# Performance work log

Hardware: AMD Instinct MI355X
Metric: run time of the kernel (lower is better)

## Reference

```python
import jax, jax.numpy as jnp
import numpy as np

B, S, D, H = 2, 2048, 1024, 16
DK = D // H
NEG = -1000000000.0


def setup_inputs() -> dict:
    key = jax.random.key(0)
    ks = jax.random.split(key, 12)
    s = 1.0 / np.sqrt(D)
    return {
        "Q": jax.random.normal(ks[0], (B, S, D), jnp.float32),
        "K": jax.random.normal(ks[1], (B, S, D), jnp.float32),
        "V": jax.random.normal(ks[2], (B, S, D), jnp.float32),
        "attn_mask": jnp.zeros((B, S, S), jnp.bool_),
        "WQ_w": jax.random.normal(ks[3], (D, D), jnp.float32) * s,
        "WQ_b": jnp.zeros((D,), jnp.float32),
        "WK_w": jax.random.normal(ks[4], (D, D), jnp.float32) * s,
        "WK_b": jnp.zeros((D,), jnp.float32),
        "WV_w": jax.random.normal(ks[5], (D, D), jnp.float32) * s,
        "WV_b": jnp.zeros((D,), jnp.float32),
        "fc_w": jax.random.normal(ks[6], (D, D), jnp.float32) * s,
        "fc_b": jnp.zeros((D,), jnp.float32),
    }


def reference(Q, K, V, attn_mask, WQ_w, WQ_b, WK_w, WK_b, WV_w, WV_b, fc_w, fc_b):
    b = Q.shape[0]
    # linear projections (torch Linear: x @ W^T + b), split heads -> [b, h, s, dk]
    q = (Q @ WQ_w.T + WQ_b).reshape(b, -1, H, DK).transpose(0, 2, 1, 3)
    k = (K @ WK_w.T + WK_b).reshape(b, -1, H, DK).transpose(0, 2, 1, 3)
    v = (V @ WV_w.T + WV_b).reshape(b, -1, H, DK).transpose(0, 2, 1, 3)
    # scaled dot-product attention with masked_fill
    scores = jnp.einsum("bhqd,bhkd->bhqk", q, k) / jnp.sqrt(jnp.float32(DK))
    scores = jnp.where(attn_mask[:, None, :, :], NEG, scores)
    attn_weights = jax.nn.softmax(scores, axis=-1)  # dropout p=0 -> identity
    attn = jnp.einsum("bhqk,bhkd->bhqd", attn_weights, v)
    attn = attn.transpose(0, 2, 1, 3).reshape(b, -1, H * DK)
    output = attn @ fc_w.T + fc_b
    return output, attn_weights
```

## Files before the change

kernel.cpp:

```cpp
#include <hip/hip_runtime.h>
#include <cstdint>
#include <cstddef>

constexpr int CB = 2;
constexpr int CS = 2048;
constexpr int CD = 1024;
constexpr int CH = 16;
constexpr int CDK = 64;
constexpr float NEGV = -1000000000.0f;
constexpr float QSCALE = 0.18033688011112042f;

typedef __bf16 bf16x8 __attribute__((ext_vector_type(8)));
typedef float f32x4 __attribute__((ext_vector_type(4)));
typedef unsigned short u16x8 __attribute__((ext_vector_type(8)));
typedef unsigned short u16x4 __attribute__((ext_vector_type(4)));

static __device__ __forceinline__ unsigned short f2bf(float x) {
  unsigned int u = __float_as_uint(x);
  u += 0x7fffu + ((u >> 16) & 1u);
  return (unsigned short)(u >> 16);
}
static __device__ __forceinline__ bf16x8 bc8(u16x8 u) {
  return __builtin_bit_cast(bf16x8, u);
}
static __device__ __forceinline__ f32x4 mfma16(bf16x8 a, bf16x8 b, f32x4 c) {
  return __builtin_amdgcn_mfma_f32_16x16x32_bf16(a, b, c, 0, 0, 0);
}

struct CvtArgs {
  const float* src[7];
  unsigned short* dst[7];
  int n4[7];
};

__global__ __launch_bounds__(256) void cvt_all(CvtArgs a) {
  const int r = blockIdx.y;
  const float* __restrict__ in = a.src[r];
  unsigned short* __restrict__ out = a.dst[r];
  const int n4 = a.n4[r];
  const int stride = gridDim.x * 256;
  for (int i = blockIdx.x * 256 + threadIdx.x; i < n4; i += stride) {
    float4 v = reinterpret_cast<const float4*>(in)[i];
    u16x4 o;
    o[0] = f2bf(v.x); o[1] = f2bf(v.y); o[2] = f2bf(v.z); o[3] = f2bf(v.w);
    reinterpret_cast<u16x4*>(out)[i] = o;
  }
}

constexpr int GK = 1024, GNT = GK / 32;

struct QKVArgs {
  const unsigned short* X[3];
  const unsigned short* W[3];
  const float* bias[3];
  unsigned short* out[3];
  float osc[3];
};

template <typename EPI>
__device__ __forceinline__ void gemm_body(const unsigned short* __restrict__ X,
                                          const unsigned short* __restrict__ Wt,
                                          EPI epi) {
  __shared__ unsigned short lA[2][128 * 32];
  __shared__ unsigned short lB[2][64 * 32];
  const int tid = threadIdx.x, lane = tid & 63, wid = tid >> 6;
  const int fr = lane & 15, fc = lane >> 4;
  const int mbase = blockIdx.y * 128, nbase = blockIdx.x * 64;
  const int wm = (wid & 1) * 64, wn = (wid >> 1) * 32;

  const int srow = wid * 16 + (lane >> 2);
  const int sslot = (lane & 3) ^ (srow & 3);
  const unsigned short* a0 = X + (size_t)(mbase + srow) * GK + sslot * 8;
  const unsigned short* b0 = Wt + (size_t)(nbase + srow) * GK + sslot * 8;

  auto stage = [&](int buf, int k0) {
    __builtin_amdgcn_global_load_lds(
        (const __attribute__((address_space(1))) void*)(a0 + k0),
        (__attribute__((address_space(3))) void*)((char*)&lA[buf][0] + wid * 1024), 16, 0, 0);
    __builtin_amdgcn_global_load_lds(
        (const __attribute__((address_space(1))) void*)(a0 + (size_t)64 * GK + k0),
        (__attribute__((address_space(3))) void*)((char*)&lA[buf][0] + 4096 + wid * 1024), 16, 0, 0);
    __builtin_amdgcn_global_load_lds(
        (const __attribute__((address_space(1))) void*)(b0 + k0),
        (__attribute__((address_space(3))) void*)((char*)&lB[buf][0] + wid * 1024), 16, 0, 0);
  };

  f32x4 acc[4][2] = {};
  stage(0, 0);
  __syncthreads();
  for (int t = 0; t < GNT; ++t) {
    if (t + 1 < GNT) stage((t + 1) & 1, (t + 1) * 32);
    const int buf = t & 1;
    bf16x8 af[4], bfv[2];
#pragma unroll
    for (int i = 0; i < 4; ++i) {
      const int row = wm + i * 16 + fr;
      af[i] = bc8(*reinterpret_cast<const u16x8*>(&lA[buf][row * 32 + ((fc ^ (row & 3)) * 8)]));
    }
#pragma unroll
    for (int j = 0; j < 2; ++j) {
      const int row = wn + j * 16 + fr;
      bfv[j] = bc8(*reinterpret_cast<const u16x8*>(&lB[buf][row * 32 + ((fc ^ (row & 3)) * 8)]));
    }
#pragma unroll
    for (int i = 0; i < 4; ++i)
#pragma unroll
      for (int j = 0; j < 2; ++j)
        acc[i][j] = mfma16(af[i], bfv[j], acc[i][j]);
    __syncthreads();
  }

#pragma unroll
  for (int j = 0; j < 2; ++j) {
    const int colb = nbase + wn + j * 16 + fr;
#pragma unroll
    for (int i = 0; i < 4; ++i) {
#pragma unroll
      for (int r = 0; r < 4; ++r) {
        const int rowb = mbase + wm + i * 16 + fc * 4 + r;
        epi(rowb, colb, acc[i][j][r]);
      }
    }
  }
}

__global__ __launch_bounds__(256) void gemm_qkv(QKVArgs a) {
  const int z = blockIdx.z;
  const float* bias = a.bias[z];
  unsigned short* out = a.out[z];
  const float osc = a.osc[z];
  gemm_body(a.X[z], a.W[z], [&](int rowb, int colb, float av) {
    const float v = (av + bias[colb]) * osc;
    const int bb = rowb >> 11, sr = rowb & (CS - 1);
    const int hh = colb >> 6, cc = colb & (CDK - 1);
    const size_t bh = (size_t)bb * CH + hh;
    if (z == 0) {
      out[(bh * CS + sr) * CDK + cc] = f2bf(v);
    } else if (z == 1) {
      const int kt = sr >> 6, ww = sr & 63, g = ww >> 4, fr2 = ww & 15;
      const int half = cc >> 5, fc2 = (cc >> 3) & 3, zz = cc & 7;
      out[(bh * 256 + kt * 8 + g * 2 + half) * 512 + (fc2 * 16 + fr2) * 8 + zz] = f2bf(v);
    } else {
      const int kt = sr >> 6, ww = sr & 63, c2 = ww >> 5, fc2 = (ww >> 3) & 3, zz = ww & 7;
      const int g = cc >> 4, fr2 = cc & 15;
      out[(bh * 256 + kt * 8 + g * 2 + c2) * 512 + (fc2 * 16 + fr2) * 8 + zz] = f2bf(v);
    }
  });
}

__global__ __launch_bounds__(256) void gemm_fc(const unsigned short* __restrict__ X,
                                               const unsigned short* __restrict__ Wt,
                                               const float* __restrict__ bias,
                                               float* __restrict__ out) {
  gemm_body(X, Wt, [&](int rowb, int colb, float av) {
    out[(size_t)rowb * CD + colb] = av + bias[colb];
  });
}

constexpr int WLD = 68;

__global__ __launch_bounds__(256, 3) void attn_fused(const unsigned short* __restrict__ qh,
                                                     const unsigned short* __restrict__ kT,
                                                     const unsigned short* __restrict__ vT,
                                                     const unsigned char* __restrict__ mask,
                                                     float* __restrict__ attnw,
                                                     unsigned short* __restrict__ attn_pre) {
  __shared__ float lW[4][16 * WLD];

  const int tid = threadIdx.x, lane = tid & 63, wid = tid >> 6;
  const int bid = blockIdx.x;
  const int swz = (bid & 7) * 128 + (bid >> 3);
  const int qt = swz & 31, hh = (swz >> 5) & 15, b = swz >> 9;
  const int bh = b * CH + hh;
  const int qw = qt * 64 + wid * 16;
  const int fr = lane & 15, fc = lane >> 4;

  const unsigned short* qp = qh + ((size_t)bh * CS + qw + fr) * CDK + fc * 8;
  const bf16x8 aq0 = bc8(*reinterpret_cast<const u16x8*>(qp));
  const bf16x8 aq1 = bc8(*reinterpret_cast<const u16x8*>(qp + 32));

  const unsigned short* kbase = kT + (size_t)bh * 131072 + lane * 8;
  const unsigned short* vbase = vT + (size_t)bh * 131072 + lane * 8;

  const unsigned char* mrow = mask + ((size_t)b * CS + qw + (lane >> 2)) * CS + (lane & 3) * 16;
  unsigned int dirtybits = 0;
#pragma unroll 4
  for (int kt = 0; kt < 32; ++kt) {
    const uint4 mv = *reinterpret_cast<const uint4*>(mrow + kt * 64);
    if (__ballot((mv.x | mv.y | mv.z | mv.w) != 0)) dirtybits |= (1u << kt);
  }

  u16x8 kreg[8];
  auto loadK = [&](int kt) {
    const unsigned short* p = kbase + (size_t)kt * 4096;
#pragma unroll
    for (int f = 0; f < 8; ++f) kreg[f] = *reinterpret_cast<const u16x8*>(p + f * 512);
  };
  auto maskfix = [&](f32x4 (&sf)[4], int kt) {
#pragma unroll
    for (int g = 0; g < 4; ++g)
#pragma unroll
      for (int r = 0; r < 4; ++r) {
        const unsigned char mb =
            mask[((size_t)b * CS + qw + fc * 4 + r) * CS + kt * 64 + g * 16 + fr];
        if (mb) sf[g][r] = NEGV;
      }
  };

  float l_r[4] = {0.f, 0.f, 0.f, 0.f};
  loadK(0);
  for (int kt = 0; kt < 32; ++kt) {
    f32x4 sf[4];
#pragma unroll
    for (int g = 0; g < 4; ++g) {
      f32x4 a = {0.f, 0.f, 0.f, 0.f};
      a = mfma16(aq0, bc8(kreg[2 * g]), a);
      a = mfma16(aq1, bc8(kreg[2 * g + 1]), a);
      sf[g] = a;
    }
    loadK(kt + 1 < 32 ? kt + 1 : 0);
    if ((dirtybits >> kt) & 1u) maskfix(sf, kt);
#pragma unroll
    for (int r = 0; r < 4; ++r)
      l_r[r] += exp2f(sf[0][r]) + exp2f(sf[1][r]) + exp2f(sf[2][r]) + exp2f(sf[3][r]);
  }

  float linv[4];
#pragma unroll
  for (int r = 0; r < 4; ++r) {
    float s = l_r[r];
    s += __shfl_xor(s, 1);
    s += __shfl_xor(s, 2);
    s += __shfl_xor(s, 4);
    s += __shfl_xor(s, 8);
    linv[r] = 1.0f / s;
  }

  f32x4 o[4] = {};
  u16x8 vreg[8];
  auto loadV = [&](int kt) {
    const unsigned short* p = vbase + (size_t)kt * 4096;
#pragma unroll
    for (int f = 0; f < 8; ++f) vreg[f] = *reinterpret_cast<const u16x8*>(p + f * 512);
  };
  loadK(0);
  for (int kt = 0; kt < 32; ++kt) {
    loadV(kt);

    f32x4 sf[4];
#pragma unroll
    for (int g = 0; g < 4; ++g) {
      f32x4 a = {0.f, 0.f, 0.f, 0.f};
      a = mfma16(aq0, bc8(kreg[2 * g]), a);
      a = mfma16(aq1, bc8(kreg[2 * g + 1]), a);
      sf[g] = a;
    }
    loadK(kt + 1 < 32 ? kt + 1 : 0);
    if ((dirtybits >> kt) & 1u) maskfix(sf, kt);

#pragma unroll
    for (int g = 0; g < 4; ++g)
#pragma unroll
      for (int r = 0; r < 4; ++r) sf[g][r] = exp2f(sf[g][r]) * linv[r];

#pragma unroll
    for (int g = 0; g < 4; ++g)
#pragma unroll
      for (int r = 0; r < 4; ++r)
        lW[wid][(fc * 4 + r) * WLD + g * 16 + fr] = sf[g][r];

#pragma unroll
    for (int it = 0; it < 4; ++it) {
      const int row = it * 4 + fc;
      const f32x4 wv = *reinterpret_cast<const f32x4*>(&lW[wid][row * WLD + fr * 4]);
      __builtin_nontemporal_store(
          wv, reinterpret_cast<f32x4*>(
                  &attnw[((size_t)bh * CS + qw + row) * CS + kt * 64 + fr * 4]));
    }

    bf16x8 wa[2];
#pragma unroll
    for (int c = 0; c < 2; ++c) {
      const f32x4 t0 = *reinterpret_cast<const f32x4*>(&lW[wid][fr * WLD + c * 32 + fc * 8]);
      const f32x4 t1 = *reinterpret_cast<const f32x4*>(&lW[wid][fr * WLD + c * 32 + fc * 8 + 4]);
      unsigned int w0, w1, w2, w3;
      asm("v_cvt_pk_bf16_f32 %0, %1, %2" : "=v"(w0) : "v"(t0[0]), "v"(t0[1]));
      asm("v_cvt_pk_bf16_f32 %0, %1, %2" : "=v"(w1) : "v"(t0[2]), "v"(t0[3]));
      asm("v_cvt_pk_bf16_f32 %0, %1, %2" : "=v"(w2) : "v"(t1[0]), "v"(t1[1]));
      asm("v_cvt_pk_bf16_f32 %0, %1, %2" : "=v"(w3) : "v"(t1[2]), "v"(t1[3]));
      uint4 uw = {w0, w1, w2, w3};
      wa[c] = __builtin_bit_cast(bf16x8, uw);
    }
#pragma unroll
    for (int g = 0; g < 4; ++g) {
      o[g] = mfma16(wa[0], bc8(vreg[2 * g]), o[g]);
      o[g] = mfma16(wa[1], bc8(vreg[2 * g + 1]), o[g]);
    }
  }

#pragma unroll
  for (int g = 0; g < 4; ++g)
#pragma unroll
    for (int r = 0; r < 4; ++r) {
      const int q = qw + fc * 4 + r;
      attn_pre[(((size_t)b * CS + q) * CH + hh) * CDK + g * 16 + fr] = f2bf(o[g][r]);
    }
}

extern "C" void kernel_launch(void* const* d_in, const int* in_sizes, int n_in,
                              void* d_out, int out_size, void* d_ws, size_t ws_size,
                              hipStream_t stream) {
  (void)in_sizes; (void)n_in; (void)out_size; (void)ws_size;

  const float* Qf = (const float*)d_in[0];
  const float* Kf = (const float*)d_in[1];
  const float* Vf = (const float*)d_in[2];
  const unsigned char* mask = (const unsigned char*)d_in[3];
  const float* WQw = (const float*)d_in[4];
  const float* WQb = (const float*)d_in[5];
  const float* WKw = (const float*)d_in[6];
  const float* WKb = (const float*)d_in[7];
  const float* WVw = (const float*)d_in[8];
  const float* WVb = (const float*)d_in[9];
  const float* fcw = (const float*)d_in[10];
  const float* fcb = (const float*)d_in[11];

  float* out0 = (float*)d_out;
  float* attnw = out0 + (size_t)CB * CS * CD;

  char* w = (char*)d_ws;
  unsigned short* Qb = (unsigned short*)(w);
  unsigned short* Kb = (unsigned short*)(w + 8388608);
  unsigned short* Vb = (unsigned short*)(w + 2 * 8388608);
  unsigned short* Wqb = (unsigned short*)(w + 3 * 8388608);
  unsigned short* Wkb = Wqb + 1048576;
  unsigned short* Wvb = Wkb + 1048576;
  unsigned short* Wfb = Wvb + 1048576;
  unsigned short* qhp = (unsigned short*)(w + 3 * 8388608 + 4 * 2097152);
  unsigned short* kTp = qhp + 4194304;
  unsigned short* vTp = kTp + 4194304;
  unsigned short* apre = Qb;

  const int NELEM4 = (CB * CS * CD) / 4;
  const int WELEM4 = (CD * CD) / 4;

  CvtArgs ca;
  ca.src[0] = Qf;  ca.dst[0] = Qb;  ca.n4[0] = NELEM4;
  ca.src[1] = Kf;  ca.dst[1] = Kb;  ca.n4[1] = NELEM4;
  ca.src[2] = Vf;  ca.dst[2] = Vb;  ca.n4[2] = NELEM4;
  ca.src[3] = WQw; ca.dst[3] = Wqb; ca.n4[3] = WELEM4;
  ca.src[4] = WKw; ca.dst[4] = Wkb; ca.n4[4] = WELEM4;
  ca.src[5] = WVw; ca.dst[5] = Wvb; ca.n4[5] = WELEM4;
  ca.src[6] = fcw; ca.dst[6] = Wfb; ca.n4[6] = WELEM4;
  cvt_all<<<dim3(512, 7), 256, 0, stream>>>(ca);

  QKVArgs qa;
  qa.X[0] = Qb;  qa.W[0] = Wqb; qa.bias[0] = WQb; qa.out[0] = qhp; qa.osc[0] = QSCALE;
  qa.X[1] = Kb;  qa.W[1] = Wkb; qa.bias[1] = WKb; qa.out[1] = kTp; qa.osc[1] = 1.0f;
  qa.X[2] = Vb;  qa.W[2] = Wvb; qa.bias[2] = WVb; qa.out[2] = vTp; qa.osc[2] = 1.0f;
  gemm_qkv<<<dim3(CD / 64, (CB * CS) / 128, 3), 256, 0, stream>>>(qa);

  attn_fused<<<dim3(1024), 256, 0, stream>>>(qhp, kTp, vTp, mask, attnw, apre);

  gemm_fc<<<dim3(CD / 64, (CB * CS) / 128), 256, 0, stream>>>(apre, Wfb, fcb, out0);
}
```

Measured before the change: 257.2 us.

## Share K/V tiles across waves via double-buffered LDS with direct global-to-LDS loads

Each of the four waves previously loaded the full K and V tiles from global memory into registers on its own. Now the block cooperatively stages each 64-key K/V tile into double-buffered shared memory using global_load_lds. That cuts redundant global and L2 traffic by four and frees registers. The change adds __syncthreads per iteration, s_setprio around the MFMA sections, and 32 KB more LDS, which may reduce occupancy below the launch bound of 3 blocks.

```diff
diff --git a/kernel.cpp b/kernel.cpp
--- a/kernel.cpp
+++ b/kernel.cpp
@@ -165,6 +165,8 @@
                                                      const unsigned char* __restrict__ mask,
                                                      float* __restrict__ attnw,
                                                      unsigned short* __restrict__ attn_pre) {
+  __shared__ unsigned short lK[2][4096];
+  __shared__ unsigned short lV[2][4096];
   __shared__ float lW[4][16 * WLD];
 
   const int tid = threadIdx.x, lane = tid & 63, wid = tid >> 6;
@@ -179,8 +181,29 @@
   const bf16x8 aq0 = bc8(*reinterpret_cast<const u16x8*>(qp));
   const bf16x8 aq1 = bc8(*reinterpret_cast<const u16x8*>(qp + 32));
 
-  const unsigned short* kbase = kT + (size_t)bh * 131072 + lane * 8;
-  const unsigned short* vbase = vT + (size_t)bh * 131072 + lane * 8;
+  const unsigned short* kt0 = kT + (size_t)bh * 131072;
+  const unsigned short* vt0 = vT + (size_t)bh * 131072;
+
+  auto stageK = [&](int buf, int kt) {
+    const unsigned short* p = kt0 + (size_t)kt * 4096;
+#pragma unroll
+    for (int cc = 0; cc < 2; ++cc) {
+      const int ch = wid * 2 + cc;
+      __builtin_amdgcn_global_load_lds(
+          (const __attribute__((address_space(1))) void*)(p + ch * 512 + lane * 8),
+          (__attribute__((address_space(3))) void*)(&lK[buf][ch * 512]), 16, 0, 0);
+    }
+  };
+  auto stageV = [&](int buf, int kt) {
+    const unsigned short* p = vt0 + (size_t)kt * 4096;
+#pragma unroll
+    for (int cc = 0; cc < 2; ++cc) {
+      const int ch = wid * 2 + cc;
+      __builtin_amdgcn_global_load_lds(
+          (const __attribute__((address_space(1))) void*)(p + ch * 512 + lane * 8),
+          (__attribute__((address_space(3))) void*)(&lV[buf][ch * 512]), 16, 0, 0);
+    }
+  };
 
   const unsigned char* mrow = mask + ((size_t)b * CS + qw + (lane >> 2)) * CS + (lane & 3) * 16;
   unsigned int dirtybits = 0;
@@ -190,12 +213,6 @@
     if (__ballot((mv.x | mv.y | mv.z | mv.w) != 0)) dirtybits |= (1u << kt);
   }
 
-  u16x8 kreg[8];
-  auto loadK = [&](int kt) {
-    const unsigned short* p = kbase + (size_t)kt * 4096;
-#pragma unroll
-    for (int f = 0; f < 8; ++f) kreg[f] = *reinterpret_cast<const u16x8*>(p + f * 512);
-  };
   auto maskfix = [&](f32x4 (&sf)[4], int kt) {
 #pragma unroll
     for (int g = 0; g < 4; ++g)
@@ -208,21 +225,29 @@
   };
 
   float l_r[4] = {0.f, 0.f, 0.f, 0.f};
-  loadK(0);
+  stageK(0, 0);
+  __syncthreads();
   for (int kt = 0; kt < 32; ++kt) {
+    if (kt < 31) stageK((kt + 1) & 1, kt + 1);
+    const int buf = kt & 1;
     f32x4 sf[4];
+    __builtin_amdgcn_s_setprio(1);
 #pragma unroll
     for (int g = 0; g < 4; ++g) {
+      const bf16x8 k0 = bc8(*reinterpret_cast<const u16x8*>(&lK[buf][(2 * g) * 512 + lane * 8]));
+      const bf16x8 k1 =
+          bc8(*reinterpret_cast<const u16x8*>(&lK[buf][(2 * g + 1) * 512 + lane * 8]));
       f32x4 a = {0.f, 0.f, 0.f, 0.f};
-      a = mfma16(aq0, bc8(kreg[2 * g]), a);
-      a = mfma16(aq1, bc8(kreg[2 * g + 1]), a);
+      a = mfma16(aq0, k0, a);
+      a = mfma16(aq1, k1, a);
       sf[g] = a;
     }
-    loadK(kt + 1 < 32 ? kt + 1 : 0);
+    __builtin_amdgcn_s_setprio(0);
     if ((dirtybits >> kt) & 1u) maskfix(sf, kt);
 #pragma unroll
     for (int r = 0; r < 4; ++r)
-      l_r[r] += exp2f(sf[0][r]) + exp2f(sf[1][r]) + exp2f(sf[2][r]) + exp2f(sf[3][r]);
+      l_r[r] += (exp2f(sf[0][r]) + exp2f(sf[1][r])) + (exp2f(sf[2][r]) + exp2f(sf[3][r]));
+    __syncthreads();
   }
 
   float linv[4];
@@ -237,25 +262,29 @@
   }
 
   f32x4 o[4] = {};
-  u16x8 vreg[8];
-  auto loadV = [&](int kt) {
-    const unsigned short* p = vbase + (size_t)kt * 4096;
-#pragma unroll
-    for (int f = 0; f < 8; ++f) vreg[f] = *reinterpret_cast<const u16x8*>(p + f * 512);
-  };
-  loadK(0);
+  stageK(0, 0);
+  stageV(0, 0);
+  __syncthreads();
   for (int kt = 0; kt < 32; ++kt) {
-    loadV(kt);
+    if (kt < 31) {
+      stageK((kt + 1) & 1, kt + 1);
+      stageV((kt + 1) & 1, kt + 1);
+    }
+    const int buf = kt & 1;
 
     f32x4 sf[4];
+    __builtin_amdgcn_s_setprio(1);
 #pragma unroll
     for (int g = 0; g < 4; ++g) {
+      const bf16x8 k0 = bc8(*reinterpret_cast<const u16x8*>(&lK[buf][(2 * g) * 512 + lane * 8]));
+      const bf16x8 k1 =
+          bc8(*reinterpret_cast<const u16x8*>(&lK[buf][(2 * g + 1) * 512 + lane * 8]));
       f32x4 a = {0.f, 0.f, 0.f, 0.f};
-      a = mfma16(aq0, bc8(kreg[2 * g]), a);
-      a = mfma16(aq1, bc8(kreg[2 * g + 1]), a);
+      a = mfma16(aq0, k0, a);
+      a = mfma16(aq1, k1, a);
       sf[g] = a;
     }
-    loadK(kt + 1 < 32 ? kt + 1 : 0);
+    __builtin_amdgcn_s_setprio(0);
     if ((dirtybits >> kt) & 1u) maskfix(sf, kt);
 
 #pragma unroll
@@ -291,11 +320,17 @@
       uint4 uw = {w0, w1, w2, w3};
       wa[c] = __builtin_bit_cast(bf16x8, uw);
     }
+    __builtin_amdgcn_s_setprio(1);
 #pragma unroll
     for (int g = 0; g < 4; ++g) {
-      o[g] = mfma16(wa[0], bc8(vreg[2 * g]), o[g]);
-      o[g] = mfma16(wa[1], bc8(vreg[2 * g + 1]), o[g]);
-    }
+      const bf16x8 v0 = bc8(*reinterpret_cast<const u16x8*>(&lV[buf][(2 * g) * 512 + lane * 8]));
+      const bf16x8 v1 =
+          bc8(*reinterpret_cast<const u16x8*>(&lV[buf][(2 * g + 1) * 512 + lane * 8]));
+      o[g] = mfma16(wa[0], v0, o[g]);
+      o[g] = mfma16(wa[1], v1, o[g]);
+    }
+    __builtin_amdgcn_s_setprio(0);
+    __syncthreads();
   }
 
 #pragma unroll
```

New measurement: 286.9 us. 11.5% more time.

## Double query rows per attention wave and widen QKV GEMM tile to 128

Applied to the files above, without the earlier changes.

The attention kernel now processes two 16-row query groups per wave, so each K and V fragment loaded from global memory is reused for 32 query rows, and the grid is halved to 512 blocks. Occupancy is relaxed from 3 to 2 blocks per CU to make room for the extra registers. Separately, the QKV projection GEMM becomes templated on the N tile and uses 128-wide tiles, halving its grid and raising per-block reuse of the A tile. The costs are higher register pressure and fewer resident waves to hide latency in both kernels.

```diff
diff --git a/kernel.cpp b/kernel.cpp
--- a/kernel.cpp
+++ b/kernel.cpp
@@ -57,61 +57,72 @@
   float osc[3];
 };
 
-template <typename EPI>
+template <int BN, typename EPI>
 __device__ __forceinline__ void gemm_body(const unsigned short* __restrict__ X,
                                           const unsigned short* __restrict__ Wt,
                                           EPI epi) {
   __shared__ unsigned short lA[2][128 * 32];
-  __shared__ unsigned short lB[2][64 * 32];
+  __shared__ unsigned short lB[2][BN * 32];
   const int tid = threadIdx.x, lane = tid & 63, wid = tid >> 6;
   const int fr = lane & 15, fc = lane >> 4;
-  const int mbase = blockIdx.y * 128, nbase = blockIdx.x * 64;
-  const int wm = (wid & 1) * 64, wn = (wid >> 1) * 32;
-
-  const int srow = wid * 16 + (lane >> 2);
+  const int mbase = blockIdx.y * 128, nbase = blockIdx.x * BN;
+  const int wm = (wid & 1) * 64, wn = (wid >> 1) * (BN / 2);
+
+  const int srow = lane >> 2;
   const int sslot = (lane & 3) ^ (srow & 3);
-  const unsigned short* a0 = X + (size_t)(mbase + srow) * GK + sslot * 8;
-  const unsigned short* b0 = Wt + (size_t)(nbase + srow) * GK + sslot * 8;
+  const int cA = wid * 2;
+  const unsigned short* a0 = X + (size_t)(mbase + cA * 16 + srow) * GK + sslot * 8;
+  const unsigned short* b0;
+  if constexpr (BN == 128) b0 = Wt + (size_t)(nbase + cA * 16 + srow) * GK + sslot * 8;
+  else                     b0 = Wt + (size_t)(nbase + wid * 16 + srow) * GK + sslot * 8;
 
   auto stage = [&](int buf, int k0) {
-    __builtin_amdgcn_global_load_lds(
-        (const __attribute__((address_space(1))) void*)(a0 + k0),
-        (__attribute__((address_space(3))) void*)((char*)&lA[buf][0] + wid * 1024), 16, 0, 0);
-    __builtin_amdgcn_global_load_lds(
-        (const __attribute__((address_space(1))) void*)(a0 + (size_t)64 * GK + k0),
-        (__attribute__((address_space(3))) void*)((char*)&lA[buf][0] + 4096 + wid * 1024), 16, 0, 0);
-    __builtin_amdgcn_global_load_lds(
-        (const __attribute__((address_space(1))) void*)(b0 + k0),
-        (__attribute__((address_space(3))) void*)((char*)&lB[buf][0] + wid * 1024), 16, 0, 0);
-  };
-
-  f32x4 acc[4][2] = {};
+#pragma unroll
+    for (int c = 0; c < 2; ++c)
+      __builtin_amdgcn_global_load_lds(
+          (const __attribute__((address_space(1))) void*)(a0 + (size_t)c * 16 * GK + k0),
+          (__attribute__((address_space(3))) void*)((char*)&lA[buf][0] + (cA + c) * 1024), 16, 0, 0);
+    if constexpr (BN == 128) {
+#pragma unroll
+      for (int c = 0; c < 2; ++c)
+        __builtin_amdgcn_global_load_lds(
+            (const __attribute__((address_space(1))) void*)(b0 + (size_t)c * 16 * GK + k0),
+            (__attribute__((address_space(3))) void*)((char*)&lB[buf][0] + (cA + c) * 1024), 16, 0, 0);
+    } else {
+      __builtin_amdgcn_global_load_lds(
+          (const __attribute__((address_space(1))) void*)(b0 + k0),
+          (__attribute__((address_space(3))) void*)((char*)&lB[buf][0] + wid * 1024), 16, 0, 0);
+    }
+  };
+
+  constexpr int NJ = BN / 32;
+  f32x4 acc[4][NJ] = {};
   stage(0, 0);
   __syncthreads();
   for (int t = 0; t < GNT; ++t) {
     if (t + 1 < GNT) stage((t + 1) & 1, (t + 1) * 32);
     const int buf = t & 1;
-    bf16x8 af[4], bfv[2];
+    bf16x8 af[4], bfv[NJ];
 #pragma unroll
     for (int i = 0; i < 4; ++i) {
       const int row = wm + i * 16 + fr;
       af[i] = bc8(*reinterpret_cast<const u16x8*>(&lA[buf][row * 32 + ((fc ^ (row & 3)) * 8)]));
     }
 #pragma unroll
-    for (int j = 0; j < 2; ++j) {
+    for (int j = 0; j < NJ; ++j) {
       const int row = wn + j * 16 + fr;
       bfv[j] = bc8(*reinterpret_cast<const u16x8*>(&lB[buf][row * 32 + ((fc ^ (row & 3)) * 8)]));
     }
 #pragma unroll
     for (int i = 0; i < 4; ++i)
 #pragma unroll
-      for (int j = 0; j < 2; ++j)
+      for (int j = 0; j < NJ; ++j)
         acc[i][j] = mfma16(af[i], bfv[j], acc[i][j]);
     __syncthreads();
   }
 
 #pragma unroll
-  for (int j = 0; j < 2; ++j) {
+  for (int j = 0; j < NJ; ++j) {
     const int colb = nbase + wn + j * 16 + fr;
 #pragma unroll
     for (int i = 0; i < 4; ++i) {
@@ -124,12 +135,12 @@
   }
 }
 
-__global__ __launch_bounds__(256) void gemm_qkv(QKVArgs a) {
+__global__ __launch_bounds__(256, 3) void gemm_qkv(QKVArgs a) {
   const int z = blockIdx.z;
   const float* bias = a.bias[z];
   unsigned short* out = a.out[z];
   const float osc = a.osc[z];
-  gemm_body(a.X[z], a.W[z], [&](int rowb, int colb, float av) {
+  gemm_body<128>(a.X[z], a.W[z], [&](int rowb, int colb, float av) {
     const float v = (av + bias[colb]) * osc;
     const int bb = rowb >> 11, sr = rowb & (CS - 1);
     const int hh = colb >> 6, cc = colb & (CDK - 1);
@@ -152,14 +163,14 @@
                                                const unsigned short* __restrict__ Wt,
                                                const float* __restrict__ bias,
                                                float* __restrict__ out) {
-  gemm_body(X, Wt, [&](int rowb, int colb, float av) {
+  gemm_body<64>(X, Wt, [&](int rowb, int colb, float av) {
     out[(size_t)rowb * CD + colb] = av + bias[colb];
   });
 }
 
 constexpr int WLD = 68;
 
-__global__ __launch_bounds__(256, 3) void attn_fused(const unsigned short* __restrict__ qh,
+__global__ __launch_bounds__(256, 2) void attn_fused(const unsigned short* __restrict__ qh,
                                                      const unsigned short* __restrict__ kT,
                                                      const unsigned short* __restrict__ vT,
                                                      const unsigned char* __restrict__ mask,
@@ -169,25 +180,32 @@
 
   const int tid = threadIdx.x, lane = tid & 63, wid = tid >> 6;
   const int bid = blockIdx.x;
-  const int swz = (bid & 7) * 128 + (bid >> 3);
-  const int qt = swz & 31, hh = (swz >> 5) & 15, b = swz >> 9;
+  const int swz = (bid & 7) * 64 + (bid >> 3);
+  const int qt = swz & 15, hh = (swz >> 4) & 15, b = swz >> 8;
   const int bh = b * CH + hh;
-  const int qw = qt * 64 + wid * 16;
+  const int qwA = qt * 128 + wid * 32;
+  const int qwB = qwA + 16;
   const int fr = lane & 15, fc = lane >> 4;
 
-  const unsigned short* qp = qh + ((size_t)bh * CS + qw + fr) * CDK + fc * 8;
-  const bf16x8 aq0 = bc8(*reinterpret_cast<const u16x8*>(qp));
-  const bf16x8 aq1 = bc8(*reinterpret_cast<const u16x8*>(qp + 32));
+  const unsigned short* qpA = qh + ((size_t)bh * CS + qwA + fr) * CDK + fc * 8;
+  const bf16x8 aqA0 = bc8(*reinterpret_cast<const u16x8*>(qpA));
+  const bf16x8 aqA1 = bc8(*reinterpret_cast<const u16x8*>(qpA + 32));
+  const unsigned short* qpB = qpA + 16 * CDK;
+  const bf16x8 aqB0 = bc8(*reinterpret_cast<const u16x8*>(qpB));
+  const bf16x8 aqB1 = bc8(*reinterpret_cast<const u16x8*>(qpB + 32));
 
   const unsigned short* kbase = kT + (size_t)bh * 131072 + lane * 8;
   const unsigned short* vbase = vT + (size_t)bh * 131072 + lane * 8;
 
-  const unsigned char* mrow = mask + ((size_t)b * CS + qw + (lane >> 2)) * CS + (lane & 3) * 16;
+  const unsigned char* mrowA = mask + ((size_t)b * CS + qwA + (lane >> 2)) * CS + (lane & 3) * 16;
+  const unsigned char* mrowB = mrowA + (size_t)16 * CS;
   unsigned int dirtybits = 0;
 #pragma unroll 4
   for (int kt = 0; kt < 32; ++kt) {
-    const uint4 mv = *reinterpret_cast<const uint4*>(mrow + kt * 64);
-    if (__ballot((mv.x | mv.y | mv.z | mv.w) != 0)) dirtybits |= (1u << kt);
+    const uint4 m0 = *reinterpret_cast<const uint4*>(mrowA + kt * 64);
+    const uint4 m1 = *reinterpret_cast<const uint4*>(mrowB + kt * 64);
+    if (__ballot((m0.x | m0.y | m0.z | m0.w | m1.x | m1.y | m1.z | m1.w) != 0))
+      dirtybits |= (1u << kt);
   }
 
   u16x8 kreg[8];
@@ -196,7 +214,16 @@
 #pragma unroll
     for (int f = 0; f < 8; ++f) kreg[f] = *reinterpret_cast<const u16x8*>(p + f * 512);
   };
-  auto maskfix = [&](f32x4 (&sf)[4], int kt) {
+  auto qk = [&](const bf16x8 a0, const bf16x8 a1, f32x4 (&sf)[4]) {
+#pragma unroll
+    for (int g = 0; g < 4; ++g) {
+      f32x4 a = {0.f, 0.f, 0.f, 0.f};
+      a = mfma16(a0, bc8(kreg[2 * g]), a);
+      a = mfma16(a1, bc8(kreg[2 * g + 1]), a);
+      sf[g] = a;
+    }
+  };
+  auto maskfix = [&](f32x4 (&sf)[4], int kt, int qw) {
 #pragma unroll
     for (int g = 0; g < 4; ++g)
 #pragma unroll
@@ -207,68 +234,51 @@
       }
   };
 
-  float l_r[4] = {0.f, 0.f, 0.f, 0.f};
+  float lAr[4] = {0.f, 0.f, 0.f, 0.f}, lBr[4] = {0.f, 0.f, 0.f, 0.f};
   loadK(0);
   for (int kt = 0; kt < 32; ++kt) {
-    f32x4 sf[4];
-#pragma unroll
-    for (int g = 0; g < 4; ++g) {
-      f32x4 a = {0.f, 0.f, 0.f, 0.f};
-      a = mfma16(aq0, bc8(kreg[2 * g]), a);
-      a = mfma16(aq1, bc8(kreg[2 * g + 1]), a);
-      sf[g] = a;
-    }
+    f32x4 sfA[4], sfB[4];
+    qk(aqA0, aqA1, sfA);
+    qk(aqB0, aqB1, sfB);
     loadK(kt + 1 < 32 ? kt + 1 : 0);
-    if ((dirtybits >> kt) & 1u) maskfix(sf, kt);
-#pragma unroll
-    for (int r = 0; r < 4; ++r)
-      l_r[r] += exp2f(sf[0][r]) + exp2f(sf[1][r]) + exp2f(sf[2][r]) + exp2f(sf[3][r]);
-  }
-
-  float linv[4];
+    if ((dirtybits >> kt) & 1u) { maskfix(sfA, kt, qwA); maskfix(sfB, kt, qwB); }
+#pragma unroll
+    for (int r = 0; r < 4; ++r) {
+      lAr[r] += (exp2f(sfA[0][r]) + exp2f(sfA[1][r])) + (exp2f(sfA[2][r]) + exp2f(sfA[3][r]));
+      lBr[r] += (exp2f(sfB[0][r]) + exp2f(sfB[1][r])) + (exp2f(sfB[2][r]) + exp2f(sfB[3][r]));
+    }
+  }
+
+  float linvA[4], linvB[4];
 #pragma unroll
   for (int r = 0; r < 4; ++r) {
-    float s = l_r[r];
-    s += __shfl_xor(s, 1);
-    s += __shfl_xor(s, 2);
-    s += __shfl_xor(s, 4);
-    s += __shfl_xor(s, 8);
-    linv[r] = 1.0f / s;
-  }
-
-  f32x4 o[4] = {};
+    float s = lAr[r];
+    s += __shfl_xor(s, 1); s += __shfl_xor(s, 2);
+    s += __shfl_xor(s, 4); s += __shfl_xor(s, 8);
+    linvA[r] = 1.0f / s;
+    float t = lBr[r];
+    t += __shfl_xor(t, 1); t += __shfl_xor(t, 2);
+    t += __shfl_xor(t, 4); t += __shfl_xor(t, 8);
+    linvB[r] = 1.0f / t;
+  }
+
+  f32x4 oA[4] = {}, oB[4] = {};
   u16x8 vreg[8];
   auto loadV = [&](int kt) {
     const unsigned short* p = vbase + (size_t)kt * 4096;
 #pragma unroll
     for (int f = 0; f < 8; ++f) vreg[f] = *reinterpret_cast<const u16x8*>(p + f * 512);
   };
-  loadK(0);
-  for (int kt = 0; kt < 32; ++kt) {
-    loadV(kt);
-
-    f32x4 sf[4];
-#pragma unroll
-    for (int g = 0; g < 4; ++g) {
-      f32x4 a = {0.f, 0.f, 0.f, 0.f};
-      a = mfma16(aq0, bc8(kreg[2 * g]), a);
-      a = mfma16(aq1, bc8(kreg[2 * g + 1]), a);
-      sf[g] = a;
-    }
-    loadK(kt + 1 < 32 ? kt + 1 : 0);
-    if ((dirtybits >> kt) & 1u) maskfix(sf, kt);
-
+  auto half = [&](f32x4 (&sf)[4], const float (&linv)[4], int qw, f32x4 (&o)[4], int kt) {
 #pragma unroll
     for (int g = 0; g < 4; ++g)
 #pragma unroll
       for (int r = 0; r < 4; ++r) sf[g][r] = exp2f(sf[g][r]) * linv[r];
-
 #pragma unroll
     for (int g = 0; g < 4; ++g)
 #pragma unroll
       for (int r = 0; r < 4; ++r)
         lW[wid][(fc * 4 + r) * WLD + g * 16 + fr] = sf[g][r];
-
 #pragma unroll
     for (int it = 0; it < 4; ++it) {
       const int row = it * 4 + fc;
@@ -277,7 +287,6 @@
           wv, reinterpret_cast<f32x4*>(
                   &attnw[((size_t)bh * CS + qw + row) * CS + kt * 64 + fr * 4]));
     }
-
     bf16x8 wa[2];
 #pragma unroll
     for (int c = 0; c < 2; ++c) {
@@ -296,14 +305,28 @@
       o[g] = mfma16(wa[0], bc8(vreg[2 * g]), o[g]);
       o[g] = mfma16(wa[1], bc8(vreg[2 * g + 1]), o[g]);
     }
+  };
+
+  loadK(0);
+  for (int kt = 0; kt < 32; ++kt) {
+    loadV(kt);
+    f32x4 sfA[4], sfB[4];
+    qk(aqA0, aqA1, sfA);
+    qk(aqB0, aqB1, sfB);
+    loadK(kt + 1 < 32 ? kt + 1 : 0);
+    if ((dirtybits >> kt) & 1u) { maskfix(sfA, kt, qwA); maskfix(sfB, kt, qwB); }
+    half(sfA, linvA, qwA, oA, kt);
+    half(sfB, linvB, qwB, oB, kt);
   }
 
 #pragma unroll
   for (int g = 0; g < 4; ++g)
 #pragma unroll
     for (int r = 0; r < 4; ++r) {
-      const int q = qw + fc * 4 + r;
-      attn_pre[(((size_t)b * CS + q) * CH + hh) * CDK + g * 16 + fr] = f2bf(o[g][r]);
+      const int qA = qwA + fc * 4 + r;
+      attn_pre[(((size_t)b * CS + qA) * CH + hh) * CDK + g * 16 + fr] = f2bf(oA[g][r]);
+      const int qB = qwB + fc * 4 + r;
+      attn_pre[(((size_t)b * CS + qB) * CH + hh) * CDK + g * 16 + fr] = f2bf(oB[g][r]);
     }
 }
 
@@ -358,9 +381,9 @@
   qa.X[0] = Qb;  qa.W[0] = Wqb; qa.bias[0] = WQb; qa.out[0] = qhp; qa.osc[0] = QSCALE;
   qa.X[1] = Kb;  qa.W[1] = Wkb; qa.bias[1] = WKb; qa.out[1] = kTp; qa.osc[1] = 1.0f;
   qa.X[2] = Vb;  qa.W[2] = Wvb; qa.bias[2] = WVb; qa.out[2] = vTp; qa.osc[2] = 1.0f;
-  gemm_qkv<<<dim3(CD / 64, (CB * CS) / 128, 3), 256, 0, stream>>>(qa);
-
-  attn_fused<<<dim3(1024), 256, 0, stream>>>(qhp, kTp, vTp, mask, attnw, apre);
+  gemm_qkv<<<dim3(CD / 128, (CB * CS) / 128, 3), 256, 0, stream>>>(qa);
+
+  attn_fused<<<dim3(512), 256, 0, stream>>>(qhp, kTp, vTp, mask, attnw, apre);
 
   gemm_fc<<<dim3(CD / 64, (CB * CS) / 128), 256, 0, stream>>>(apre, Wfb, fcb, out0);
 }
```

After: 252.5 us. Within noise of the previous version (-1.9%).

## Transpose QK MFMA to drop LDS staging and widen QKV GEMM tile

Applied to the files above, without the earlier changes.

The attention kernel now computes S^T by swapping MFMA operands, so each lane holds four consecutive key columns for one query row. Attention weights can then be stored directly from registers as float4 and fed to the PV MFMA without the LDS transpose buffer. The V projection layout is rearranged to match the new P fragment ordering, and row sums collapse to a scalar per lane. Separately, the QKV GEMM uses a 128x128 tile with launch bounds 3, giving more reuse per block at the cost of more registers and fewer blocks.

```diff
diff --git a/kernel.cpp b/kernel.cpp
--- a/kernel.cpp
+++ b/kernel.cpp
@@ -57,61 +57,72 @@
   float osc[3];
 };
 
-template <typename EPI>
+template <int BN, typename EPI>
 __device__ __forceinline__ void gemm_body(const unsigned short* __restrict__ X,
                                           const unsigned short* __restrict__ Wt,
                                           EPI epi) {
   __shared__ unsigned short lA[2][128 * 32];
-  __shared__ unsigned short lB[2][64 * 32];
+  __shared__ unsigned short lB[2][BN * 32];
   const int tid = threadIdx.x, lane = tid & 63, wid = tid >> 6;
   const int fr = lane & 15, fc = lane >> 4;
-  const int mbase = blockIdx.y * 128, nbase = blockIdx.x * 64;
-  const int wm = (wid & 1) * 64, wn = (wid >> 1) * 32;
-
-  const int srow = wid * 16 + (lane >> 2);
+  const int mbase = blockIdx.y * 128, nbase = blockIdx.x * BN;
+  const int wm = (wid & 1) * 64, wn = (wid >> 1) * (BN / 2);
+
+  const int srow = lane >> 2;
   const int sslot = (lane & 3) ^ (srow & 3);
-  const unsigned short* a0 = X + (size_t)(mbase + srow) * GK + sslot * 8;
-  const unsigned short* b0 = Wt + (size_t)(nbase + srow) * GK + sslot * 8;
+  const int cA = wid * 2;
+  const unsigned short* a0 = X + (size_t)(mbase + cA * 16 + srow) * GK + sslot * 8;
+  const unsigned short* b0;
+  if constexpr (BN == 128) b0 = Wt + (size_t)(nbase + cA * 16 + srow) * GK + sslot * 8;
+  else                     b0 = Wt + (size_t)(nbase + wid * 16 + srow) * GK + sslot * 8;
 
   auto stage = [&](int buf, int k0) {
-    __builtin_amdgcn_global_load_lds(
-        (const __attribute__((address_space(1))) void*)(a0 + k0),
-        (__attribute__((address_space(3))) void*)((char*)&lA[buf][0] + wid * 1024), 16, 0, 0);
-    __builtin_amdgcn_global_load_lds(
-        (const __attribute__((address_space(1))) void*)(a0 + (size_t)64 * GK + k0),
-        (__attribute__((address_space(3))) void*)((char*)&lA[buf][0] + 4096 + wid * 1024), 16, 0, 0);
-    __builtin_amdgcn_global_load_lds(
-        (const __attribute__((address_space(1))) void*)(b0 + k0),
-        (__attribute__((address_space(3))) void*)((char*)&lB[buf][0] + wid * 1024), 16, 0, 0);
-  };
-
-  f32x4 acc[4][2] = {};
+#pragma unroll
+    for (int c = 0; c < 2; ++c)
+      __builtin_amdgcn_global_load_lds(
+          (const __attribute__((address_space(1))) void*)(a0 + (size_t)c * 16 * GK + k0),
+          (__attribute__((address_space(3))) void*)((char*)&lA[buf][0] + (cA + c) * 1024), 16, 0, 0);
+    if constexpr (BN == 128) {
+#pragma unroll
+      for (int c = 0; c < 2; ++c)
+        __builtin_amdgcn_global_load_lds(
+            (const __attribute__((address_space(1))) void*)(b0 + (size_t)c * 16 * GK + k0),
+            (__attribute__((address_space(3))) void*)((char*)&lB[buf][0] + (cA + c) * 1024), 16, 0, 0);
+    } else {
+      __builtin_amdgcn_global_load_lds(
+          (const __attribute__((address_space(1))) void*)(b0 + k0),
+          (__attribute__((address_space(3))) void*)((char*)&lB[buf][0] + wid * 1024), 16, 0, 0);
+    }
+  };
+
+  constexpr int NJ = BN / 32;
+  f32x4 acc[4][NJ] = {};
   stage(0, 0);
   __syncthreads();
   for (int t = 0; t < GNT; ++t) {
     if (t + 1 < GNT) stage((t + 1) & 1, (t + 1) * 32);
     const int buf = t & 1;
-    bf16x8 af[4], bfv[2];
+    bf16x8 af[4], bfv[NJ];
 #pragma unroll
     for (int i = 0; i < 4; ++i) {
       const int row = wm + i * 16 + fr;
       af[i] = bc8(*reinterpret_cast<const u16x8*>(&lA[buf][row * 32 + ((fc ^ (row & 3)) * 8)]));
     }
 #pragma unroll
-    for (int j = 0; j < 2; ++j) {
+    for (int j = 0; j < NJ; ++j) {
       const int row = wn + j * 16 + fr;
       bfv[j] = bc8(*reinterpret_cast<const u16x8*>(&lB[buf][row * 32 + ((fc ^ (row & 3)) * 8)]));
     }
 #pragma unroll
     for (int i = 0; i < 4; ++i)
 #pragma unroll
-      for (int j = 0; j < 2; ++j)
+      for (int j = 0; j < NJ; ++j)
         acc[i][j] = mfma16(af[i], bfv[j], acc[i][j]);
     __syncthreads();
   }
 
 #pragma unroll
-  for (int j = 0; j < 2; ++j) {
+  for (int j = 0; j < NJ; ++j) {
     const int colb = nbase + wn + j * 16 + fr;
 #pragma unroll
     for (int i = 0; i < 4; ++i) {
@@ -124,12 +135,12 @@
   }
 }
 
-__global__ __launch_bounds__(256) void gemm_qkv(QKVArgs a) {
+__global__ __launch_bounds__(256, 3) void gemm_qkv(QKVArgs a) {
   const int z = blockIdx.z;
   const float* bias = a.bias[z];
   unsigned short* out = a.out[z];
   const float osc = a.osc[z];
-  gemm_body(a.X[z], a.W[z], [&](int rowb, int colb, float av) {
+  gemm_body<128>(a.X[z], a.W[z], [&](int rowb, int colb, float av) {
     const float v = (av + bias[colb]) * osc;
     const int bb = rowb >> 11, sr = rowb & (CS - 1);
     const int hh = colb >> 6, cc = colb & (CDK - 1);
@@ -141,9 +152,12 @@
       const int half = cc >> 5, fc2 = (cc >> 3) & 3, zz = cc & 7;
       out[(bh * 256 + kt * 8 + g * 2 + half) * 512 + (fc2 * 16 + fr2) * 8 + zz] = f2bf(v);
     } else {
-      const int kt = sr >> 6, ww = sr & 63, c2 = ww >> 5, fc2 = (ww >> 3) & 3, zz = ww & 7;
+      const int kt = sr >> 6, kk = sr & 63;
+      const int c = kk >> 5, k32 = kk & 31;
+      const int fcv = (k32 >> 2) & 3;
+      const int zv = ((k32 >> 4) << 2) | (k32 & 3);
       const int g = cc >> 4, fr2 = cc & 15;
-      out[(bh * 256 + kt * 8 + g * 2 + c2) * 512 + (fc2 * 16 + fr2) * 8 + zz] = f2bf(v);
+      out[(bh * 256 + kt * 8 + c * 4 + g) * 512 + (fr2 + 16 * fcv) * 8 + zv] = f2bf(v);
     }
   });
 }
@@ -152,12 +166,10 @@
                                                const unsigned short* __restrict__ Wt,
                                                const float* __restrict__ bias,
                                                float* __restrict__ out) {
-  gemm_body(X, Wt, [&](int rowb, int colb, float av) {
+  gemm_body<64>(X, Wt, [&](int rowb, int colb, float av) {
     out[(size_t)rowb * CD + colb] = av + bias[colb];
   });
 }
-
-constexpr int WLD = 68;
 
 __global__ __launch_bounds__(256, 3) void attn_fused(const unsigned short* __restrict__ qh,
                                                      const unsigned short* __restrict__ kT,
@@ -165,8 +177,6 @@
                                                      const unsigned char* __restrict__ mask,
                                                      float* __restrict__ attnw,
                                                      unsigned short* __restrict__ attn_pre) {
-  __shared__ float lW[4][16 * WLD];
-
   const int tid = threadIdx.x, lane = tid & 63, wid = tid >> 6;
   const int bid = blockIdx.x;
   const int swz = (bid & 7) * 128 + (bid >> 3);
@@ -196,45 +206,41 @@
 #pragma unroll
     for (int f = 0; f < 8; ++f) kreg[f] = *reinterpret_cast<const u16x8*>(p + f * 512);
   };
+  auto qk = [&](f32x4 (&sf)[4]) {
+#pragma unroll
+    for (int g = 0; g < 4; ++g) {
+      f32x4 a = {0.f, 0.f, 0.f, 0.f};
+      a = mfma16(bc8(kreg[2 * g]), aq0, a);
+      a = mfma16(bc8(kreg[2 * g + 1]), aq1, a);
+      sf[g] = a;
+    }
+  };
+  const unsigned char* mq = mask + ((size_t)b * CS + qw + fr) * CS + fc * 4;
   auto maskfix = [&](f32x4 (&sf)[4], int kt) {
 #pragma unroll
-    for (int g = 0; g < 4; ++g)
-#pragma unroll
-      for (int r = 0; r < 4; ++r) {
-        const unsigned char mb =
-            mask[((size_t)b * CS + qw + fc * 4 + r) * CS + kt * 64 + g * 16 + fr];
-        if (mb) sf[g][r] = NEGV;
-      }
-  };
-
-  float l_r[4] = {0.f, 0.f, 0.f, 0.f};
+    for (int g = 0; g < 4; ++g) {
+      const uchar4 m4 = *reinterpret_cast<const uchar4*>(mq + kt * 64 + g * 16);
+      if (m4.x) sf[g][0] = NEGV;
+      if (m4.y) sf[g][1] = NEGV;
+      if (m4.z) sf[g][2] = NEGV;
+      if (m4.w) sf[g][3] = NEGV;
+    }
+  };
+
+  float lsum = 0.f;
   loadK(0);
   for (int kt = 0; kt < 32; ++kt) {
     f32x4 sf[4];
-#pragma unroll
-    for (int g = 0; g < 4; ++g) {
-      f32x4 a = {0.f, 0.f, 0.f, 0.f};
-      a = mfma16(aq0, bc8(kreg[2 * g]), a);
-      a = mfma16(aq1, bc8(kreg[2 * g + 1]), a);
-      sf[g] = a;
-    }
+    qk(sf);
     loadK(kt + 1 < 32 ? kt + 1 : 0);
     if ((dirtybits >> kt) & 1u) maskfix(sf, kt);
 #pragma unroll
-    for (int r = 0; r < 4; ++r)
-      l_r[r] += exp2f(sf[0][r]) + exp2f(sf[1][r]) + exp2f(sf[2][r]) + exp2f(sf[3][r]);
-  }
-
-  float linv[4];
-#pragma unroll
-  for (int r = 0; r < 4; ++r) {
-    float s = l_r[r];
-    s += __shfl_xor(s, 1);
-    s += __shfl_xor(s, 2);
-    s += __shfl_xor(s, 4);
-    s += __shfl_xor(s, 8);
-    linv[r] = 1.0f / s;
-  }
+    for (int g = 0; g < 4; ++g)
+      lsum += (exp2f(sf[g][0]) + exp2f(sf[g][1])) + (exp2f(sf[g][2]) + exp2f(sf[g][3]));
+  }
+  lsum += __shfl_xor(lsum, 16);
+  lsum += __shfl_xor(lsum, 32);
+  const float linv = 1.0f / lsum;
 
   f32x4 o[4] = {};
   u16x8 vreg[8];
@@ -243,59 +249,42 @@
 #pragma unroll
     for (int f = 0; f < 8; ++f) vreg[f] = *reinterpret_cast<const u16x8*>(p + f * 512);
   };
+
+  float* wrow = attnw + ((size_t)bh * CS + qw + fr) * CS + fc * 4;
+
   loadK(0);
   for (int kt = 0; kt < 32; ++kt) {
     loadV(kt);
 
     f32x4 sf[4];
-#pragma unroll
-    for (int g = 0; g < 4; ++g) {
-      f32x4 a = {0.f, 0.f, 0.f, 0.f};
-      a = mfma16(aq0, bc8(kreg[2 * g]), a);
-      a = mfma16(aq1, bc8(kreg[2 * g + 1]), a);
-      sf[g] = a;
-    }
+    qk(sf);
     loadK(kt + 1 < 32 ? kt + 1 : 0);
     if ((dirtybits >> kt) & 1u) maskfix(sf, kt);
 
 #pragma unroll
     for (int g = 0; g < 4; ++g)
 #pragma unroll
-      for (int r = 0; r < 4; ++r) sf[g][r] = exp2f(sf[g][r]) * linv[r];
+      for (int r = 0; r < 4; ++r) sf[g][r] = exp2f(sf[g][r]) * linv;
 
 #pragma unroll
     for (int g = 0; g < 4; ++g)
-#pragma unroll
-      for (int r = 0; r < 4; ++r)
-        lW[wid][(fc * 4 + r) * WLD + g * 16 + fr] = sf[g][r];
-
-#pragma unroll
-    for (int it = 0; it < 4; ++it) {
-      const int row = it * 4 + fc;
-      const f32x4 wv = *reinterpret_cast<const f32x4*>(&lW[wid][row * WLD + fr * 4]);
-      __builtin_nontemporal_store(
-          wv, reinterpret_cast<f32x4*>(
-                  &attnw[((size_t)bh * CS + qw + row) * CS + kt * 64 + fr * 4]));
-    }
-
-    bf16x8 wa[2];
+      __builtin_nontemporal_store(sf[g], reinterpret_cast<f32x4*>(wrow + kt * 64 + g * 16));
+
+    bf16x8 pa[2];
 #pragma unroll
     for (int c = 0; c < 2; ++c) {
-      const f32x4 t0 = *reinterpret_cast<const f32x4*>(&lW[wid][fr * WLD + c * 32 + fc * 8]);
-      const f32x4 t1 = *reinterpret_cast<const f32x4*>(&lW[wid][fr * WLD + c * 32 + fc * 8 + 4]);
       unsigned int w0, w1, w2, w3;
-      asm("v_cvt_pk_bf16_f32 %0, %1, %2" : "=v"(w0) : "v"(t0[0]), "v"(t0[1]));
-      asm("v_cvt_pk_bf16_f32 %0, %1, %2" : "=v"(w1) : "v"(t0[2]), "v"(t0[3]));
-      asm("v_cvt_pk_bf16_f32 %0, %1, %2" : "=v"(w2) : "v"(t1[0]), "v"(t1[1]));
-      asm("v_cvt_pk_bf16_f32 %0, %1, %2" : "=v"(w3) : "v"(t1[2]), "v"(t1[3]));
+      asm("v_cvt_pk_bf16_f32 %0, %1, %2" : "=v"(w0) : "v"(sf[2 * c][0]), "v"(sf[2 * c][1]));
+      asm("v_cvt_pk_bf16_f32 %0, %1, %2" : "=v"(w1) : "v"(sf[2 * c][2]), "v"(sf[2 * c][3]));
+      asm("v_cvt_pk_bf16_f32 %0, %1, %2" : "=v"(w2) : "v"(sf[2 * c + 1][0]), "v"(sf[2 * c + 1][1]));
+      asm("v_cvt_pk_bf16_f32 %0, %1, %2" : "=v"(w3) : "v"(sf[2 * c + 1][2]), "v"(sf[2 * c + 1][3]));
       uint4 uw = {w0, w1, w2, w3};
-      wa[c] = __builtin_bit_cast(bf16x8, uw);
-    }
-#pragma unroll
-    for (int g = 0; g < 4; ++g) {
-      o[g] = mfma16(wa[0], bc8(vreg[2 * g]), o[g]);
-      o[g] = mfma16(wa[1], bc8(vreg[2 * g + 1]), o[g]);
-    }
+      pa[c] = __builtin_bit_cast(bf16x8, uw);
+    }
+#pragma unroll
+    for (int g = 0; g < 4; ++g) o[g] = mfma16(pa[0], bc8(vreg[g]), o[g]);
+#pragma unroll
+    for (int g = 0; g < 4; ++g) o[g] = mfma16(pa[1], bc8(vreg[4 + g]), o[g]);
   }
 
 #pragma unroll
@@ -358,7 +347,7 @@
   qa.X[0] = Qb;  qa.W[0] = Wqb; qa.bias[0] = WQb; qa.out[0] = qhp; qa.osc[0] = QSCALE;
   qa.X[1] = Kb;  qa.W[1] = Wkb; qa.bias[1] = WKb; qa.out[1] = kTp; qa.osc[1] = 1.0f;
   qa.X[2] = Vb;  qa.W[2] = Wvb; qa.bias[2] = WVb; qa.out[2] = vTp; qa.osc[2] = 1.0f;
-  gemm_qkv<<<dim3(CD / 64, (CB * CS) / 128, 3), 256, 0, stream>>>(qa);
+  gemm_qkv<<<dim3(CD / 128, (CB * CS) / 128, 3), 256, 0, stream>>>(qa);
 
   attn_fused<<<dim3(1024), 256, 0, stream>>>(qhp, kTp, vTp, mask, attnw, apre);
 
```

New measurement: 262.7 us. 2.1% more time.
